# Performance work log

Hardware: AMD Instinct MI355X
Metric: run time of the kernel (lower is better)

## Reference

```python
import jax, jax.numpy as jnp
import numpy as np

B = 4096
F_ST, F_DY, M = 20, 10, 50
E = 16
N_ST, N_DY = 100000, 1000000
F_ALL = F_ST + F_DY                      # 30 fields total
P = F_ALL * (F_ALL - 1) // 2             # 435 strict upper-triangular pairs
D_IN = P * E                             # 6960 MLP input dim
H = 512
BN_EPS = 1e-5


def _bn(x, g, b):
    # BatchNorm1d in training mode: biased batch variance (matches torch)
    m = jnp.mean(x, axis=0)
    v = jnp.var(x, axis=0)
    return g * (x - m) * jax.lax.rsqrt(v + BN_EPS) + b


def setup_inputs() -> dict:
    key = jax.random.key(0)
    ks = jax.random.split(key, 16)
    s_emb = 0.02
    inp = {
        "static_ids": jax.random.randint(ks[0], (B, F_ST), 0, N_ST),
        "dynamic_ids": jax.random.randint(ks[1], (B, F_DY, M), 0, N_DY),
        "dynamic_lengths": jax.random.randint(ks[2], (B, F_DY), 1, M + 1),
        "st_emb": jax.random.normal(ks[3], (N_ST, E), jnp.float32) * s_emb,
        "dy_emb": jax.random.normal(ks[4], (N_DY, E), jnp.float32) * s_emb,
        "st_lr": jax.random.normal(ks[5], (N_ST, 1), jnp.float32) * s_emb,
        "dy_lr": jax.random.normal(ks[6], (N_DY, 1), jnp.float32) * s_emb,
        "bias": jax.random.normal(ks[7], (1,), jnp.float32),
        "bn1_g": jnp.ones((D_IN,), jnp.float32), "bn1_b": jnp.zeros((D_IN,), jnp.float32),
        "W1": jax.random.normal(ks[8], (D_IN, H), jnp.float32) / np.sqrt(D_IN),
        "b1": jnp.zeros((H,), jnp.float32),
        "bn2_g": jnp.ones((H,), jnp.float32), "bn2_b": jnp.zeros((H,), jnp.float32),
        "W2": jax.random.normal(ks[9], (H, H), jnp.float32) / np.sqrt(H),
        "b2": jnp.zeros((H,), jnp.float32),
        "bn3_g": jnp.ones((H,), jnp.float32), "bn3_b": jnp.zeros((H,), jnp.float32),
        "W3": jax.random.normal(ks[10], (H, H), jnp.float32) / np.sqrt(H),
        "b3": jnp.zeros((H,), jnp.float32),
        "bn_out_g": jnp.ones((H,), jnp.float32), "bn_out_b": jnp.zeros((H,), jnp.float32),
        "W_out": jax.random.normal(ks[11], (H, 1), jnp.float32) / np.sqrt(H),
        "b_out": jnp.zeros((1,), jnp.float32),
    }
    return inp


def reference(static_ids, dynamic_ids, dynamic_lengths,
              st_emb, dy_emb, st_lr, dy_lr, bias,
              bn1_g, bn1_b, W1, b1,
              bn2_g, bn2_b, W2, b2,
              bn3_g, bn3_b, W3, b3,
              bn_out_g, bn_out_b, W_out, b_out):
    lengths = jnp.maximum(dynamic_lengths, 1)                       # guard avg div
    valid = (jnp.arange(M)[None, None, :] < lengths[:, :, None])    # [B,Fdy,M]
    valid_f = valid.astype(jnp.float32)

    # DyEmb (method='avg'): masked mean over list positions -> [B,Fdy,E]
    dyn_tab = dy_emb[dynamic_ids]                                   # [B,Fdy,M,E]
    dyn_embeddings = jnp.einsum('bfme,bfm->bfe', dyn_tab, valid_f) / lengths[..., None].astype(jnp.float32)
    # StEmb: plain lookup -> [B,Fst,E]
    st_embeddings = st_emb[static_ids]

    all_emb = jnp.concatenate([st_embeddings, dyn_embeddings], axis=1)  # [B,F_ALL,E]

    # Strict upper triangle pairs (static indices == the boolean mask in torch code)
    iu, ju = np.triu_indices(F_ALL, k=1)                            # each [P]
    combine = all_emb[:, iu, :] * all_emb[:, ju, :]                 # [B,P,E]
    x = combine.reshape(combine.shape[0], -1)                       # [B, P*E]

    # Linear parts: StEmb/DyEmb with embedding_size=1 (dyLr uses method='sum')
    static_lr_out = st_lr[static_ids][..., 0]                       # [B,Fst]
    dyn_lr_out = jnp.einsum('bfm,bfm->bf', dy_lr[dynamic_ids][..., 0], valid_f)  # [B,Fdy]

    # BN -> Linear -> ReLU tower
    h1 = _bn(x, bn1_g, bn1_b) @ W1 + b1
    h2 = _bn(jax.nn.relu(h1), bn2_g, bn2_b) @ W2 + b2
    out3 = _bn(jax.nn.relu(h2), bn3_g, bn3_b) @ W3 + b3             # embedding_lr_out_3
    # final BN+Linear is computed in torch but unused in scores (kept faithful)
    _ = _bn(jax.nn.relu(out3), bn_out_g, bn_out_b) @ W_out + b_out

    scores = (bias
              + jnp.sum(static_lr_out, axis=-1)
              + jnp.sum(dyn_lr_out, axis=-1)
              + jnp.sum(out3, axis=-1))                             # [B]
    return scores
```

## Files before the change

kernel.cpp:

```cpp
#include <hip/hip_runtime.h>

typedef __attribute__((ext_vector_type(8))) short short8;
typedef __attribute__((ext_vector_type(4))) float f32x4;

__device__ __forceinline__ unsigned short f2b(float f) {
    union { float f; unsigned u; } uf; uf.f = f;
    unsigned r = uf.u + 0x7fffu + ((uf.u >> 16) & 1u);
    return (unsigned short)(r >> 16);
}
__device__ __forceinline__ float b2f(unsigned short b) {
    union { unsigned u; float f; } uf; uf.u = ((unsigned)b) << 16;
    return uf.f;
}
__device__ __forceinline__ void gload_lds16(const void* g, void* l) {
    __builtin_amdgcn_global_load_lds(
        (const __attribute__((address_space(1))) void*)g,
        (__attribute__((address_space(3))) void*)l,
        16, 0, 0);
}

#define B_SZ 4096
#define F_ST 20
#define F_DY 10
#define MLEN 50
#define E_SZ 16
#define F_ALL 30
#define NPAIR 435
#define DIN 6960
#define KP 7168
#define H_SZ 512
#define BN_EPS 1e-5f

__global__ __launch_bounds__(256) void k_stemb(
    const int* __restrict__ st_ids, const float* __restrict__ st_emb,
    float* __restrict__ all_emb)
{
    int idx = blockIdx.x * 256 + threadIdx.x;
    int e4 = idx & 3, bf = idx >> 2;
    int b = bf / F_ST, f = bf % F_ST;
    int id = st_ids[bf];
    f32x4 v = *(const f32x4*)(st_emb + (long)id * E_SZ + e4 * 4);
    *(f32x4*)(all_emb + ((long)b * F_ALL + f) * E_SZ + e4 * 4) = v;
}

__global__ __launch_bounds__(512) void k_dyemb(
    const int* __restrict__ dy_ids, const int* __restrict__ dy_len,
    const float* __restrict__ dy_emb, float* __restrict__ all_emb)
{
    int gw = blockIdx.x * 8 + (threadIdx.x >> 6);
    int l = threadIdx.x & 63;
    int b = gw / F_DY, f = gw - b * F_DY;
    int len = dy_len[b * F_DY + f]; if (len < 1) len = 1;
    const int* ids = dy_ids + ((long)b * F_DY + f) * MLEN;
    int idv = (l < MLEN) ? ids[l] : 0;
    int e = l & 15, mq = l >> 4;
    float acc = 0.f;
#pragma unroll
    for (int j = 0; j < 13; ++j) {
        int m = mq + (j << 2);
        int id = __shfl(idv, m, 64);
        float v = (m < len) ? dy_emb[(long)id * E_SZ + e] : 0.f;
        acc += v;
    }
    acc += __shfl_xor(acc, 16, 64);
    acc += __shfl_xor(acc, 32, 64);
    if (l < 16)
        all_emb[((long)b * F_ALL + F_ST + f) * E_SZ + e] = acc / (float)len;
}

__global__ __launch_bounds__(512) void k_lr(
    const int* __restrict__ st_ids, const int* __restrict__ dy_ids,
    const int* __restrict__ dy_len, const float* __restrict__ st_lr,
    const float* __restrict__ dy_lr, const float* __restrict__ bias,
    float* __restrict__ lr_score)
{
    int w = threadIdx.x >> 6, l = threadIdx.x & 63;
    int b = blockIdx.x * 8 + w;
    float acc = 0.f;
    if (l < F_ST) acc += st_lr[st_ids[b * F_ST + l]];
#pragma unroll
    for (int i = 0; i < 8; ++i) {
        int idx = i * 64 + l;
        if (idx < F_DY * MLEN) {
            int f = idx / MLEN, m = idx - f * MLEN;
            int len = dy_len[b * F_DY + f]; if (len < 1) len = 1;
            if (m < len)
                acc += dy_lr[dy_ids[((long)b * F_DY + f) * MLEN + m]];
        }
    }
    for (int s = 32; s; s >>= 1) acc += __shfl_down(acc, s, 64);
    if (l == 0) lr_score[b] = bias[0] + acc;
}

__global__ __launch_bounds__(1024) void k_x(
    const float* __restrict__ all_emb, unsigned short* __restrict__ x16,
    float* __restrict__ s1, float* __restrict__ s1q)
{
    __shared__ float es[16 * 480];
    __shared__ int pip[NPAIR], pjp[NPAIR];
    int t = threadIdx.x, b0 = blockIdx.x * 16;
    if (t < NPAIR) {
        int i = 0, rem = t;
        while (rem >= (F_ALL - 1) - i) { rem -= (F_ALL - 1) - i; ++i; }
        pip[t] = i; pjp[t] = i + 1 + rem;
    }
    for (int idx = t; idx < 16 * 480; idx += 1024)
        es[idx] = all_emb[(long)b0 * 480 + idx];
    __syncthreads();

    int ci[7], cj[7];
#pragma unroll
    for (int k = 0; k < 7; ++k) {
        int d = t + (k << 10);
        if (d < DIN) {
            int p = d >> 4, e = d & 15;
            ci[k] = pip[p] * E_SZ + e;
            cj[k] = pjp[p] * E_SZ + e;
        } else { ci[k] = -1; cj[k] = 0; }
    }
    float sum[7], sq[7];
#pragma unroll
    for (int k = 0; k < 7; ++k) { sum[k] = 0.f; sq[k] = 0.f; }

    for (int r = 0; r < 16; ++r) {
        const float* row = &es[r * 480];
        long ob = (long)(b0 + r) * KP;
#pragma unroll
        for (int k = 0; k < 7; ++k) {
            int d = t + (k << 10);
            if (ci[k] >= 0) {
                float v = row[ci[k]] * row[cj[k]];
                unsigned short h = f2b(v);
                x16[ob + d] = h;
                float vb = b2f(h);
                sum[k] += vb; sq[k] += vb * vb;
            } else if (d < KP) {
                x16[ob + d] = 0;
            }
        }
    }
#pragma unroll
    for (int k = 0; k < 7; ++k) {
        int d = t + (k << 10);
        if (ci[k] >= 0) { atomicAdd(&s1[d], sum[k]); atomicAdd(&s1q[d], sq[k]); }
    }
}

__global__ __launch_bounds__(256) void k_prep(
    const float* __restrict__ s, const float* __restrict__ sqs,
    const float* __restrict__ g, const float* __restrict__ bb,
    float* __restrict__ a, float* __restrict__ c,
    const float* __restrict__ W3, float* __restrict__ w3s)
{
    int t = threadIdx.x;
    if (blockIdx.x < 28) {
        int d = blockIdx.x * 256 + t;
        if (d < DIN) {
            float m = s[d] * (1.f / 4096.f);
            float var = sqs[d] * (1.f / 4096.f) - m * m;
            float av = g[d] * rsqrtf(var + BN_EPS);
            a[d] = av; c[d] = bb[d] - m * av;
        }
    } else {
        int row = (blockIdx.x - 28) * 16 + (t >> 4), sub = t & 15;
        float acc = 0.f;
        for (int i = 0; i < 32; ++i) acc += W3[(long)row * H_SZ + sub + i * 16];
#pragma unroll
        for (int sh = 8; sh; sh >>= 1) acc += __shfl_xor(acc, sh, 16);
        if (sub == 0) w3s[row] = acc;
    }
}

__global__ __launch_bounds__(256) void k_w1t(
    const float* __restrict__ W1, const float* __restrict__ a1,
    const float* __restrict__ c1, unsigned short* __restrict__ w1t,
    float* __restrict__ con)
{
    int gi = blockIdx.x * 256 + threadIdx.x;
    int kg = gi >> 9, n = gi & 511;
    short8 out; float cacc = 0.f;
#pragma unroll
    for (int i = 0; i < 8; ++i) {
        int k = kg * 8 + i;
        if (k < DIN) {
            float w = W1[(long)k * H_SZ + n];
            out[i] = (short)f2b(a1[k] * w);
            cacc += c1[k] * w;
        } else out[i] = 0;
    }
    *(short8*)(w1t + (long)n * KP + kg * 8) = out;
    atomicAdd(&con[n], cacc);
}

template <int PS>
__device__ __forceinline__ void gemm1_body(
    const unsigned short* __restrict__ A, const unsigned short* __restrict__ Bt,
    float* __restrict__ p0, float* __restrict__ p1,
    float* __restrict__ p2, float* __restrict__ p3)
{
    __shared__ __align__(16) short As[64 * 64];
    __shared__ __align__(16) short Bs[256 * 64];
    const int t = threadIdx.x;
    const int w = t >> 6, l = t & 63;
    const int lm = l & 15, lq = l >> 4;
    const int s = blockIdx.x;
    const int combo = s & 7;
    const int nb = combo & 1;
    const int z = combo >> 1;
    const int row0 = (s >> 3) * 64;
    const int k0 = z * (KP / 4);
    const int col_base = nb * 256;

    const int srow = t >> 3;
    const int gch = (t & 7) ^ (srow & 7);
    const unsigned short* gA = A + (long)(row0 + srow) * KP + k0 + gch * 8;
    const unsigned short* gB = Bt + (long)(col_base + srow) * KP + k0 + gch * 8;
    short* AsW = As + w * 512;
    short* BsW = Bs + w * 512;

    f32x4 acc[4][2];
#pragma unroll
    for (int mi = 0; mi < 4; ++mi)
#pragma unroll
        for (int ni = 0; ni < 2; ++ni) acc[mi][ni] = (f32x4){0.f,0.f,0.f,0.f};

    for (int kt = 0; kt < 28; ++kt) {
        gload_lds16(gA, AsW);
#pragma unroll
        for (int c = 0; c < 4; ++c)
            gload_lds16(gB + (long)(64 * c) * KP, BsW + c * 4096);
        __syncthreads();
#pragma unroll
        for (int sb = 0; sb < 2; ++sb) {
            short8 af[4];
#pragma unroll
            for (int mi = 0; mi < 4; ++mi) {
                int m = mi * 16 + lm;
                int sl = (sb * 4 + lq) ^ (m & 7);
                af[mi] = *(const short8*)(As + m * 64 + sl * 8);
            }
#pragma unroll
            for (int ni = 0; ni < 2; ++ni) {
                int rb = w * 32 + ni * 16 + lm;
                int sl = (sb * 4 + lq) ^ (rb & 7);
                short8 bf = *(const short8*)(Bs + rb * 64 + sl * 8);
#pragma unroll
                for (int mi = 0; mi < 4; ++mi)
                    acc[mi][ni] = __builtin_amdgcn_mfma_f32_16x16x32_bf16(
                        af[mi], bf, acc[mi][ni], 0, 0, 0);
            }
        }
        __syncthreads();
        gA += 64; gB += 64;
    }

    float* pz;
    if (PS) pz = (z == 0) ? p0 : (z == 1) ? p1 : (z == 2) ? p2 : p3;
    else    pz = p0;
#pragma unroll
    for (int ni = 0; ni < 2; ++ni) {
        int col = col_base + w * 32 + ni * 16 + lm;
#pragma unroll
        for (int mi = 0; mi < 4; ++mi) {
            int rbase = row0 + mi * 16 + lq * 4;
#pragma unroll
            for (int r = 0; r < 4; ++r) {
                long idx = (long)(rbase + r) * H_SZ + col;
                if (PS) pz[idx] = acc[mi][ni][r];
                else    atomicAdd(&pz[idx], acc[mi][ni][r]);
            }
        }
    }
}

__global__ __launch_bounds__(512, 4) void k_gemm1_ps(
    const unsigned short* __restrict__ A, const unsigned short* __restrict__ Bt,
    float* __restrict__ p0, float* __restrict__ p1,
    float* __restrict__ p2, float* __restrict__ p3)
{ gemm1_body<1>(A, Bt, p0, p1, p2, p3); }

__global__ __launch_bounds__(512, 4) void k_gemm1_at(
    const unsigned short* __restrict__ A, const unsigned short* __restrict__ Bt,
    float* __restrict__ accbuf)
{ gemm1_body<0>(A, Bt, accbuf, accbuf, accbuf, accbuf); }

template <int PS>
__device__ __forceinline__ void ep_body(
    const float* __restrict__ p0, const float* __restrict__ p1,
    const float* __restrict__ p2, const float* __restrict__ p3,
    const float* __restrict__ con1, const float* __restrict__ b1,
    unsigned short* __restrict__ r1, float* __restrict__ s2,
    float* __restrict__ s2q)
{
    __shared__ float con[H_SZ];
    int t = threadIdx.x, r0 = blockIdx.x * 32;
    con[t] = b1[t] + con1[t];
    con[t + 256] = b1[t + 256] + con1[t + 256];
    __syncthreads();
    float a0 = 0.f, q0 = 0.f, a1v = 0.f, q1 = 0.f;
    for (int r = 0; r < 32; ++r) {
        long base = (long)(r0 + r) * H_SZ;
        float v0, v1;
        if (PS) {
            v0 = p0[base + t] + p1[base + t] + p2[base + t] + p3[base + t]
               + con[t];
            v1 = p0[base + t + 256] + p1[base + t + 256]
               + p2[base + t + 256] + p3[base + t + 256] + con[t + 256];
        } else {
            v0 = p0[base + t] + con[t];
            v1 = p0[base + t + 256] + con[t + 256];
        }
        v0 = v0 > 0.f ? v0 : 0.f;
        v1 = v1 > 0.f ? v1 : 0.f;
        unsigned short h0 = f2b(v0), h1 = f2b(v1);
        r1[base + t] = h0; r1[base + t + 256] = h1;
        float b0 = b2f(h0), b1f = b2f(h1);
        a0 += b0; q0 += b0 * b0; a1v += b1f; q1 += b1f * b1f;
    }
    atomicAdd(&s2[t], a0);        atomicAdd(&s2q[t], q0);
    atomicAdd(&s2[t + 256], a1v); atomicAdd(&s2q[t + 256], q1);
}

__global__ __launch_bounds__(256) void k_ep_ps(
    const float* __restrict__ p0, const float* __restrict__ p1,
    const float* __restrict__ p2, const float* __restrict__ p3,
    const float* __restrict__ con1, const float* __restrict__ b1,
    unsigned short* __restrict__ r1, float* __restrict__ s2,
    float* __restrict__ s2q)
{ ep_body<1>(p0, p1, p2, p3, con1, b1, r1, s2, s2q); }

__global__ __launch_bounds__(256) void k_ep_at(
    const float* __restrict__ accbuf,
    const float* __restrict__ con1, const float* __restrict__ b1,
    unsigned short* __restrict__ r1, float* __restrict__ s2,
    float* __restrict__ s2q)
{ ep_body<0>(accbuf, accbuf, accbuf, accbuf, con1, b1, r1, s2, s2q); }

__global__ __launch_bounds__(256) void k_w2t(
    const float* __restrict__ W2, const float* __restrict__ s2,
    const float* __restrict__ s2q, const float* __restrict__ g2,
    const float* __restrict__ bb2, unsigned short* __restrict__ w2t,
    float* __restrict__ con)
{
    int gi = blockIdx.x * 256 + threadIdx.x;
    int kg = gi >> 9, n = gi & 511;
    short8 out; float cacc = 0.f;
#pragma unroll
    for (int i = 0; i < 8; ++i) {
        int k = kg * 8 + i;
        float m = s2[k] * (1.f / 4096.f);
        float var = s2q[k] * (1.f / 4096.f) - m * m;
        float av = g2[k] * rsqrtf(var + BN_EPS);
        float cv = bb2[k] - m * av;
        float w = W2[(long)k * H_SZ + n];
        out[i] = (short)f2b(av * w);
        cacc += cv * w;
    }
    *(short8*)(w2t + (long)n * H_SZ + kg * 8) = out;
    atomicAdd(&con[n], cacc);
}

__global__ __launch_bounds__(512) void k_gemm2(
    const unsigned short* __restrict__ A, const unsigned short* __restrict__ Bt,
    const float* __restrict__ cvec, const float* __restrict__ bvec,
    unsigned short* __restrict__ Out, float* __restrict__ ss,
    float* __restrict__ sq)
{
    const int Kp = H_SZ;
    __shared__ __align__(16) short As[2][128 * 32];
    __shared__ __align__(16) short Bs[2][64 * 32];
    const int t = threadIdx.x;
    const int w = t >> 6, l = t & 63;
    const int wm = w >> 1, wn = w & 1;
    const int lm = l & 15, lq = l >> 4;
    const int row0 = blockIdx.y * 128;
    const int col0 = blockIdx.x * 64;

    const unsigned short* gA = A + (long)(row0 + (t >> 2)) * Kp + ((t & 3) * 8);
    const unsigned short* gB = Bt + (long)(col0 + ((t >> 2) & 63)) * Kp + ((t & 3) * 8);

#define STAGE2(kt, pb) do {                                                   \
        gload_lds16(gA + (kt) * 32, &As[pb][w * 512]);                        \
        if (t < 256) gload_lds16(gB + (kt) * 32, &Bs[pb][w * 512]);           \
    } while (0)

    f32x4 acc00 = {0.f,0.f,0.f,0.f}, acc01 = acc00, acc10 = acc00, acc11 = acc00;

    STAGE2(0, 0);
    __syncthreads();

    for (int kt = 0; kt < Kp / 32; ++kt) {
        const int pb = kt & 1;
        if (kt < Kp / 32 - 1) STAGE2(kt + 1, pb ^ 1);
        const short* aBase0 = &As[pb][(wm * 32 + lm) * 32 + lq * 8];
        const short* bBase0 = &Bs[pb][(wn * 32 + lm) * 32 + lq * 8];
        short8 af0 = *(const short8*)aBase0;
        short8 af1 = *(const short8*)(aBase0 + 16 * 32);
        short8 bf0 = *(const short8*)bBase0;
        short8 bf1 = *(const short8*)(bBase0 + 16 * 32);
        acc00 = __builtin_amdgcn_mfma_f32_16x16x32_bf16(af0, bf0, acc00, 0, 0, 0);
        acc01 = __builtin_amdgcn_mfma_f32_16x16x32_bf16(af0, bf1, acc01, 0, 0, 0);
        acc10 = __builtin_amdgcn_mfma_f32_16x16x32_bf16(af1, bf0, acc10, 0, 0, 0);
        acc11 = __builtin_amdgcn_mfma_f32_16x16x32_bf16(af1, bf1, acc11, 0, 0, 0);
        __syncthreads();
    }
#undef STAGE2

    f32x4 accs[2][2] = {{acc00, acc01}, {acc10, acc11}};
#pragma unroll
    for (int ni = 0; ni < 2; ++ni) {
        int col = col0 + wn * 32 + ni * 16 + lm;
        float cb = cvec[col] + bvec[col];
        float psum = 0.f, psq = 0.f;
#pragma unroll
        for (int mi = 0; mi < 2; ++mi) {
            int rbase = row0 + wm * 32 + mi * 16 + lq * 4;
#pragma unroll
            for (int r = 0; r < 4; ++r) {
                float v = accs[mi][ni][r] + cb;
                v = v > 0.f ? v : 0.f;
                unsigned short h = f2b(v);
                Out[(long)(rbase + r) * H_SZ + col] = h;
                float vb = b2f(h);
                psum += vb; psq += vb * vb;
            }
        }
        psum += __shfl_xor(psum, 16, 64); psum += __shfl_xor(psum, 32, 64);
        psq  += __shfl_xor(psq , 16, 64); psq  += __shfl_xor(psq , 32, 64);
        if (lq == 0) { atomicAdd(&ss[col], psum); atomicAdd(&sq[col], psq); }
    }
}

__global__ __launch_bounds__(256) void k_final(
    const unsigned short* __restrict__ r2, const float* __restrict__ s3,
    const float* __restrict__ s3q, const float* __restrict__ g3,
    const float* __restrict__ bb3, const float* __restrict__ w3s,
    const float* __restrict__ b3, const float* __restrict__ lr_score,
    float* __restrict__ out)
{
    int t = threadIdx.x, w = t >> 6, l = t & 63;
    int b = blockIdx.x * 4 + w;
    float acc = 0.f;
#pragma unroll
    for (int i = 0; i < 8; ++i) {
        int e = i * 64 + l;
        float m = s3[e] * (1.f / 4096.f);
        float var = s3q[e] * (1.f / 4096.f) - m * m;
        float a3 = g3[e] * rsqrtf(var + BN_EPS);
        float c3 = bb3[e] - m * a3;
        float v = a3 * b2f(r2[(long)b * H_SZ + e]) + c3;
        acc += v * w3s[e] + b3[e];
    }
    for (int s = 32; s; s >>= 1) acc += __shfl_down(acc, s, 64);
    if (l == 0) out[b] = lr_score[b] + acc;
}

extern "C" void kernel_launch(void* const* d_in, const int* in_sizes, int n_in,
                              void* d_out, int out_size, void* d_ws, size_t ws_size,
                              hipStream_t stream) {
    const int*   st_ids = (const int*)d_in[0];
    const int*   dy_ids = (const int*)d_in[1];
    const int*   dy_len = (const int*)d_in[2];
    const float* st_emb = (const float*)d_in[3];
    const float* dy_emb = (const float*)d_in[4];
    const float* st_lr  = (const float*)d_in[5];
    const float* dy_lr  = (const float*)d_in[6];
    const float* bias   = (const float*)d_in[7];
    const float* bn1_g  = (const float*)d_in[8];
    const float* bn1_b  = (const float*)d_in[9];
    const float* W1     = (const float*)d_in[10];
    const float* b1     = (const float*)d_in[11];
    const float* bn2_g  = (const float*)d_in[12];
    const float* bn2_b  = (const float*)d_in[13];
    const float* W2     = (const float*)d_in[14];
    const float* b2     = (const float*)d_in[15];
    const float* bn3_g  = (const float*)d_in[16];
    const float* bn3_b  = (const float*)d_in[17];
    const float* W3     = (const float*)d_in[18];
    const float* b3     = (const float*)d_in[19];

    char* ws = (char*)d_ws;
    size_t off = 0;
    auto alloc = [&](size_t bytes) -> char* {
        char* p = ws + off;
        off = (off + bytes + 255) & ~(size_t)255;
        return p;
    };
    char* R = alloc((size_t)B_SZ * H_SZ * 4);
    float*          all_emb = (float*)R;
    float*          accbuf  = (float*)R;
    unsigned short* r2      = (unsigned short*)R;

    unsigned short* x16     = (unsigned short*)alloc((size_t)B_SZ * KP * 2);
    unsigned short* w1t     = (unsigned short*)alloc((size_t)H_SZ * KP * 2);
    unsigned short* r1      = (unsigned short*)alloc((size_t)B_SZ * H_SZ * 2);
    unsigned short* w2t     = (unsigned short*)alloc((size_t)H_SZ * H_SZ * 2);
    float*          lr_sc   = (float*)alloc(B_SZ * 4);
    float* a1  = (float*)alloc(KP * 4);
    float* c1  = (float*)alloc(KP * 4);
    float* w3s = (float*)alloc(H_SZ * 4);
    char* zstart = ws + off;
    float* s1   = (float*)alloc(KP * 4);
    float* s1q  = (float*)alloc(KP * 4);
    float* con1 = (float*)alloc(H_SZ * 4);
    float* s2   = (float*)alloc(H_SZ * 4);
    float* s2q  = (float*)alloc(H_SZ * 4);
    float* con2 = (float*)alloc(H_SZ * 4);
    float* s3   = (float*)alloc(H_SZ * 4);
    float* s3q  = (float*)alloc(H_SZ * 4);
    size_t zbytes = (size_t)((ws + off) - zstart);

    float* pb1 = (float*)alloc((size_t)B_SZ * H_SZ * 4);
    float* pb2 = (float*)alloc((size_t)B_SZ * H_SZ * 4);
    float* pb3 = (float*)alloc((size_t)B_SZ * H_SZ * 4);
    const bool ps = (off <= ws_size);

    hipMemsetAsync(zstart, 0, zbytes, stream);
    k_stemb<<<(B_SZ * F_ST * 4) / 256, 256, 0, stream>>>(st_ids, st_emb, all_emb);
    k_dyemb<<<(B_SZ * F_DY) / 8, 512, 0, stream>>>(dy_ids, dy_len, dy_emb, all_emb);
    k_lr<<<B_SZ / 8, 512, 0, stream>>>(st_ids, dy_ids, dy_len, st_lr, dy_lr,
                                       bias, lr_sc);
    k_x<<<B_SZ / 16, 1024, 0, stream>>>(all_emb, x16, s1, s1q);
    k_prep<<<60, 256, 0, stream>>>(s1, s1q, bn1_g, bn1_b, a1, c1, W3, w3s);
    k_w1t<<<(896 * 512) / 256, 256, 0, stream>>>(W1, a1, c1, w1t, con1);
    if (ps) {
        k_gemm1_ps<<<512, 512, 0, stream>>>(x16, w1t, accbuf, pb1, pb2, pb3);
        k_ep_ps<<<128, 256, 0, stream>>>(accbuf, pb1, pb2, pb3, con1, b1,
                                         r1, s2, s2q);
    } else {
        hipMemsetAsync(R, 0, (size_t)B_SZ * H_SZ * 4, stream);
        k_gemm1_at<<<512, 512, 0, stream>>>(x16, w1t, accbuf);
        k_ep_at<<<128, 256, 0, stream>>>(accbuf, con1, b1, r1, s2, s2q);
    }
    k_w2t<<<128, 256, 0, stream>>>(W2, s2, s2q, bn2_g, bn2_b, w2t, con2);
    k_gemm2<<<dim3(8, 32), 512, 0, stream>>>(r1, w2t, con2, b2, r2, s3, s3q);
    k_final<<<B_SZ / 4, 256, 0, stream>>>(r2, s3, s3q, bn3_g, bn3_b, w3s, b3,
                                          lr_sc, (float*)d_out);
}
```

Before: 325.2 us.

## Fuse static embedding gather and linear-term scoring into existing kernels

Removes the separate static-embedding and LR-score kernels. The static gather now happens inside the pairwise-product kernel, writing straight to shared memory, and dynamic LR sums are accumulated in the dynamic-embedding kernel through atomics into a zeroed buffer. This cuts two launches and the global round-trip for static embeddings. In exchange it adds atomics, and the order of floating-point summation in the linear score changes.

```diff
diff --git a/kernel.cpp b/kernel.cpp
--- a/kernel.cpp
+++ b/kernel.cpp
@@ -31,21 +31,10 @@
 #define H_SZ 512
 #define BN_EPS 1e-5f
 
-__global__ __launch_bounds__(256) void k_stemb(
-    const int* __restrict__ st_ids, const float* __restrict__ st_emb,
-    float* __restrict__ all_emb)
-{
-    int idx = blockIdx.x * 256 + threadIdx.x;
-    int e4 = idx & 3, bf = idx >> 2;
-    int b = bf / F_ST, f = bf % F_ST;
-    int id = st_ids[bf];
-    f32x4 v = *(const f32x4*)(st_emb + (long)id * E_SZ + e4 * 4);
-    *(f32x4*)(all_emb + ((long)b * F_ALL + f) * E_SZ + e4 * 4) = v;
-}
-
 __global__ __launch_bounds__(512) void k_dyemb(
     const int* __restrict__ dy_ids, const int* __restrict__ dy_len,
-    const float* __restrict__ dy_emb, float* __restrict__ all_emb)
+    const float* __restrict__ dy_emb, const float* __restrict__ dy_lr,
+    float* __restrict__ all_emb, float* __restrict__ lr_sc)
 {
     int gw = blockIdx.x * 8 + (threadIdx.x >> 6);
     int l = threadIdx.x & 63;
@@ -54,59 +43,58 @@
     const int* ids = dy_ids + ((long)b * F_DY + f) * MLEN;
     int idv = (l < MLEN) ? ids[l] : 0;
     int e = l & 15, mq = l >> 4;
-    float acc = 0.f;
+    float acc = 0.f, lac = 0.f;
 #pragma unroll
     for (int j = 0; j < 13; ++j) {
         int m = mq + (j << 2);
         int id = __shfl(idv, m, 64);
-        float v = (m < len) ? dy_emb[(long)id * E_SZ + e] : 0.f;
+        bool p = (m < len);
+        float v = p ? dy_emb[(long)id * E_SZ + e] : 0.f;
         acc += v;
+        if (e == 0) lac += p ? dy_lr[id] : 0.f;
     }
     acc += __shfl_xor(acc, 16, 64);
     acc += __shfl_xor(acc, 32, 64);
+    lac += __shfl_xor(lac, 16, 64);
+    lac += __shfl_xor(lac, 32, 64);
+    if (l == 0) atomicAdd(&lr_sc[b], lac);
     if (l < 16)
         all_emb[((long)b * F_ALL + F_ST + f) * E_SZ + e] = acc / (float)len;
 }
 
-__global__ __launch_bounds__(512) void k_lr(
-    const int* __restrict__ st_ids, const int* __restrict__ dy_ids,
-    const int* __restrict__ dy_len, const float* __restrict__ st_lr,
-    const float* __restrict__ dy_lr, const float* __restrict__ bias,
-    float* __restrict__ lr_score)
-{
-    int w = threadIdx.x >> 6, l = threadIdx.x & 63;
-    int b = blockIdx.x * 8 + w;
-    float acc = 0.f;
-    if (l < F_ST) acc += st_lr[st_ids[b * F_ST + l]];
-#pragma unroll
-    for (int i = 0; i < 8; ++i) {
-        int idx = i * 64 + l;
-        if (idx < F_DY * MLEN) {
-            int f = idx / MLEN, m = idx - f * MLEN;
-            int len = dy_len[b * F_DY + f]; if (len < 1) len = 1;
-            if (m < len)
-                acc += dy_lr[dy_ids[((long)b * F_DY + f) * MLEN + m]];
-        }
-    }
-    for (int s = 32; s; s >>= 1) acc += __shfl_down(acc, s, 64);
-    if (l == 0) lr_score[b] = bias[0] + acc;
-}
-
 __global__ __launch_bounds__(1024) void k_x(
+    const int* __restrict__ st_ids, const float* __restrict__ st_emb,
+    const float* __restrict__ st_lr, const float* __restrict__ bias,
     const float* __restrict__ all_emb, unsigned short* __restrict__ x16,
-    float* __restrict__ s1, float* __restrict__ s1q)
+    float* __restrict__ s1, float* __restrict__ s1q,
+    float* __restrict__ lr_sc)
 {
     __shared__ float es[16 * 480];
     __shared__ int pip[NPAIR], pjp[NPAIR];
+    __shared__ float lrs[16];
     int t = threadIdx.x, b0 = blockIdx.x * 16;
+    if (t < 16) lrs[t] = 0.f;
     if (t < NPAIR) {
         int i = 0, rem = t;
         while (rem >= (F_ALL - 1) - i) { rem -= (F_ALL - 1) - i; ++i; }
         pip[t] = i; pjp[t] = i + 1 + rem;
     }
-    for (int idx = t; idx < 16 * 480; idx += 1024)
-        es[idx] = all_emb[(long)b0 * 480 + idx];
     __syncthreads();
+
+    for (int i = t; i < 16 * F_ST * 4; i += 1024) {
+        int e4 = i & 3, bf = i >> 2;
+        int r = bf / F_ST, f = bf - r * F_ST;
+        int id = st_ids[(b0 + r) * F_ST + f];
+        f32x4 v = *(const f32x4*)(st_emb + (long)id * E_SZ + e4 * 4);
+        *(f32x4*)(&es[r * 480 + f * 16 + e4 * 4]) = v;
+        if (e4 == 0) atomicAdd(&lrs[r], st_lr[id]);
+    }
+    for (int i = t; i < 16 * 160; i += 1024) {
+        int r = i / 160, j = i - r * 160;
+        es[r * 480 + 320 + j] = all_emb[((long)(b0 + r) * 480) + 320 + j];
+    }
+    __syncthreads();
+    if (t < 16) atomicAdd(&lr_sc[b0 + t], lrs[t] + bias[0]);
 
     int ci[7], cj[7];
 #pragma unroll
@@ -495,7 +483,6 @@
     unsigned short* w1t     = (unsigned short*)alloc((size_t)H_SZ * KP * 2);
     unsigned short* r1      = (unsigned short*)alloc((size_t)B_SZ * H_SZ * 2);
     unsigned short* w2t     = (unsigned short*)alloc((size_t)H_SZ * H_SZ * 2);
-    float*          lr_sc   = (float*)alloc(B_SZ * 4);
     float* a1  = (float*)alloc(KP * 4);
     float* c1  = (float*)alloc(KP * 4);
     float* w3s = (float*)alloc(H_SZ * 4);
@@ -508,6 +495,7 @@
     float* con2 = (float*)alloc(H_SZ * 4);
     float* s3   = (float*)alloc(H_SZ * 4);
     float* s3q  = (float*)alloc(H_SZ * 4);
+    float* lr_sc = (float*)alloc(B_SZ * 4);
     size_t zbytes = (size_t)((ws + off) - zstart);
 
     float* pb1 = (float*)alloc((size_t)B_SZ * H_SZ * 4);
@@ -516,11 +504,10 @@
     const bool ps = (off <= ws_size);
 
     hipMemsetAsync(zstart, 0, zbytes, stream);
-    k_stemb<<<(B_SZ * F_ST * 4) / 256, 256, 0, stream>>>(st_ids, st_emb, all_emb);
-    k_dyemb<<<(B_SZ * F_DY) / 8, 512, 0, stream>>>(dy_ids, dy_len, dy_emb, all_emb);
-    k_lr<<<B_SZ / 8, 512, 0, stream>>>(st_ids, dy_ids, dy_len, st_lr, dy_lr,
-                                       bias, lr_sc);
-    k_x<<<B_SZ / 16, 1024, 0, stream>>>(all_emb, x16, s1, s1q);
+    k_dyemb<<<(B_SZ * F_DY) / 8, 512, 0, stream>>>(dy_ids, dy_len, dy_emb,
+                                                   dy_lr, all_emb, lr_sc);
+    k_x<<<B_SZ / 16, 1024, 0, stream>>>(st_ids, st_emb, st_lr, bias,
+                                        all_emb, x16, s1, s1q, lr_sc);
     k_prep<<<60, 256, 0, stream>>>(s1, s1q, bn1_g, bn1_b, a1, c1, W3, w3s);
     k_w1t<<<(896 * 512) / 256, 256, 0, stream>>>(W1, a1, c1, w1t, con1);
     if (ps) {
```

New measurement: 335.4 us. +3.1%, slower.
